# Optimization experiments

Hardware: AMD Instinct MI355X
Metric: run time of the kernel (lower is better)

## Reference

```python
import jax, jax.numpy as jnp
import numpy as np

TAU = 1.0
EPS = 1e-8  # F.cosine_similarity eps


def _cl(X, Y):
    # Pairwise cosine similarity via L2-normalize + single GEMM (N,D)@(D,N)
    Xn = X / jnp.maximum(jnp.linalg.norm(X, axis=1, keepdims=True), EPS)
    Yn = Y / jnp.maximum(jnp.linalg.norm(Y, axis=1, keepdims=True), EPS)
    sim = Xn @ Yn.T  # [N, N], sim[i, j] = cos(X_i, Y_j)
    e = jnp.exp(sim / TAU)
    pos = jnp.diagonal(e)               # exp(diag(sim)/tau), [N]
    neg = jnp.sum(e, axis=0) - pos      # column sums minus positive, [N]
    return -jnp.log(pos / neg).reshape(X.shape[0], 1)


def setup_inputs() -> dict:
    key = jax.random.key(0)
    ks = jax.random.split(key, 6)
    N, D1, D2, DO = 8192, 1024, 768, 256
    X = jax.random.normal(ks[0], (N, D1), dtype=jnp.float32)
    Y = jax.random.normal(ks[1], (N, D2), dtype=jnp.float32)
    # nn.Linear params (kaiming-uniform-ish scale)
    Wx = jax.random.uniform(ks[2], (DO, D1), jnp.float32, -1, 1) / np.sqrt(D1)
    bx = jax.random.uniform(ks[3], (DO,), jnp.float32, -1, 1) / np.sqrt(D1)
    Wy = jax.random.uniform(ks[4], (DO, D2), jnp.float32, -1, 1) / np.sqrt(D2)
    by = jax.random.uniform(ks[5], (DO,), jnp.float32, -1, 1) / np.sqrt(D2)
    return {"X": X, "Y": Y, "Wx": Wx, "bx": bx, "Wy": Wy, "by": by}


def reference(X, Y, Wx, bx, Wy, by):
    Xp = X @ Wx.T + bx  # proj_x
    Yp = Y @ Wy.T + by  # proj_y
    return _cl(Xp, Yp) + _cl(Yp, Xp)  # [N, 1]
```

## Files before the change

kernel.cpp:

```cpp
#include <hip/hip_runtime.h>
#include <hip/hip_bf16.h>

typedef __bf16 bf16_t;
typedef __bf16 bf16x8 __attribute__((ext_vector_type(8)));
typedef float  f32x4  __attribute__((ext_vector_type(4)));
typedef int    i32x8  __attribute__((ext_vector_type(8)));

__device__ __forceinline__ bf16x8 pack8(f32x4 a, f32x4 b) {
    bf16x8 h = { (bf16_t)a.x, (bf16_t)a.y, (bf16_t)a.z, (bf16_t)a.w,
                 (bf16_t)b.x, (bf16_t)b.y, (bf16_t)b.z, (bf16_t)b.w };
    return h;
}

__device__ __forceinline__ void gl_lds16(const void* g, void* l) {
    __builtin_amdgcn_global_load_lds(
        (const __attribute__((address_space(1))) unsigned int*)g,
        (__attribute__((address_space(3))) unsigned int*)l, 16, 0, 0);
}

#if __has_builtin(__builtin_amdgcn_cvt_pk_fp8_f32)
__device__ __forceinline__ unsigned char cvt1_e4m3(float x) {
    return (unsigned char)(__builtin_amdgcn_cvt_pk_fp8_f32(x, x, 0, false) & 0xff);
}
#else
__device__ __forceinline__ unsigned char cvt1_e4m3(float x) {
    unsigned u = __float_as_uint(x);
    unsigned sign = (u >> 24) & 0x80u;
    float a = fabsf(x);
    if (a < 7.8125e-3f) { int q = (int)(a * 512.0f + 0.5f); return (unsigned char)(sign | q); }
    if (a >= 448.0f) return (unsigned char)(sign | 0x7E);
    unsigned au = u & 0x7FFFFFFFu;
    unsigned lsb = (au >> 20) & 1u;
    au += 0x7FFFFu + lsb;
    int exp = (int)(au >> 23) - 127;
    unsigned man = (au >> 20) & 7u;
    return (unsigned char)(sign | ((unsigned)(exp + 7) << 3) | man);
}
#endif

__device__ __forceinline__ int frag_off_k(int row16, int k) {
    return ((k >> 6) << 10) + (((k >> 3) & 3) << 8) + (row16 << 4)
         + (((k >> 5) & 1) << 3) + (k & 7);
}

__global__ __launch_bounds__(256) void wconv(
    const float* __restrict__ Wx, const float* __restrict__ Wy,
    bf16_t* __restrict__ Wxt, bf16_t* __restrict__ Wyt)
{
    int id = blockIdx.x * 256 + threadIdx.x;

    int row, k0, K;
    const float* W;
    bf16_t* Wt;
    if (id < 32768) { W = Wx; Wt = Wxt; K = 1024; row = id >> 7; k0 = (id & 127) << 3; }
    else { int c = id - 32768; W = Wy; Wt = Wyt; K = 768; row = c / 96; k0 = (c % 96) << 3; }

    f32x4 lo = *reinterpret_cast<const f32x4*>(&W[(size_t)row * K + k0]);
    f32x4 hi = *reinterpret_cast<const f32x4*>(&W[(size_t)row * K + k0 + 4]);
    size_t off = (size_t)(row >> 4) * 16 * K + frag_off_k(row & 15, k0);
    *reinterpret_cast<bf16x8*>(Wt + off) = pack8(lo, hi);
}

__global__ __launch_bounds__(512, 2) void proj_norm(
    const float* __restrict__ X, const float* __restrict__ Y,
    const bf16_t* __restrict__ Wxt, const float* __restrict__ bxp,
    const bf16_t* __restrict__ Wyt, const float* __restrict__ byp,
    unsigned char* __restrict__ Xt, unsigned char* __restrict__ Yt)
{
    __shared__ float Abuf[2][64 * 64];
    __shared__ unsigned char obuf[16384];
    __shared__ float ssqL[4][64];

    const int tid  = threadIdx.x;
    const int lane = tid & 63;
    const int wave = tid >> 6;
    const int quad = lane >> 4;
    const int c16  = lane & 15;
    const int rg   = wave >> 2;
    const int cg   = wave & 3;

    const bool isY = blockIdx.x >= 128;
    const float*  A    = isY ? Y   : X;
    const bf16_t* Wt   = isY ? Wyt : Wxt;
    const float*  bias = isY ? byp : bxp;
    unsigned char* dst = isY ? Yt  : Xt;
    const int K = isY ? 768 : 1024;
    const int S = K >> 6;
    const int rowBase = (blockIdx.x & 127) * 64;

    auto stage = [&](int s, int b) {
        #pragma unroll
        for (int t = 0; t < 2; ++t) {
            int r0  = (wave * 2 + t) * 4;
            int row = r0 + (lane >> 4);
            int gch = (lane & 15) ^ (row & 15);
            gl_lds16(&A[(size_t)(rowBase + row) * K + s * 64 + gch * 4],
                     &Abuf[b][r0 * 64]);
        }
    };

    auto aFrag = [&](int b, int mf, int s2) -> bf16x8 {
        int row = rg * 32 + mf * 16 + c16;
        int e   = s2 * 8 + quad * 2;
        const float* base = &Abuf[b][row * 64];
        f32x4 lo = *reinterpret_cast<const f32x4*>(base + ((e ^ c16) << 2));
        f32x4 hi = *reinterpret_cast<const f32x4*>(base + (((e + 1) ^ c16) << 2));
        return pack8(lo, hi);
    };

    const bf16_t* pB[4];
    #pragma unroll
    for (int nf = 0; nf < 4; ++nf)
        pB[nf] = Wt + (size_t)(cg * 4 + nf) * 16 * K + quad * 256 + c16 * 16;

    f32x4 acc[2][4] = {};
    stage(0, 0);

    for (int s = 0; s < S; ++s) {
        const int b = s & 1;
        __syncthreads();
        if (s + 1 < S) stage(s + 1, b ^ 1);
        #pragma unroll
        for (int s2 = 0; s2 < 2; ++s2) {
            bf16x8 bF[4];
            #pragma unroll
            for (int nf = 0; nf < 4; ++nf)
                bF[nf] = *reinterpret_cast<const bf16x8*>(pB[nf] + s * 1024 + s2 * 8);
            #pragma unroll
            for (int mf = 0; mf < 2; ++mf) {
                bf16x8 aF = aFrag(b, mf, s2);
                #pragma unroll
                for (int nf = 0; nf < 4; ++nf)
                    acc[mf][nf] = __builtin_amdgcn_mfma_f32_16x16x32_bf16(
                        aF, bF[nf], acc[mf][nf], 0, 0, 0);
            }
        }
    }

    #pragma unroll
    for (int nf = 0; nf < 4; ++nf) {
        float bb = bias[cg * 64 + nf * 16 + c16];
        #pragma unroll
        for (int mf = 0; mf < 2; ++mf)
            #pragma unroll
            for (int r = 0; r < 4; ++r) acc[mf][nf][r] += bb;
    }

    #pragma unroll
    for (int mf = 0; mf < 2; ++mf)
        #pragma unroll
        for (int r = 0; r < 4; ++r) {
            float v = 0.f;
            #pragma unroll
            for (int nf = 0; nf < 4; ++nf) v += acc[mf][nf][r] * acc[mf][nf][r];
            v += __shfl_xor(v, 1, 64);
            v += __shfl_xor(v, 2, 64);
            v += __shfl_xor(v, 4, 64);
            v += __shfl_xor(v, 8, 64);
            if (c16 == 0) ssqL[cg][rg * 32 + mf * 16 + quad * 4 + r] = v;
        }
    __syncthreads();

    #pragma unroll
    for (int mf = 0; mf < 2; ++mf)
        #pragma unroll
        for (int r = 0; r < 4; ++r) {
            int lr = rg * 32 + mf * 16 + quad * 4 + r;
            float t = ssqL[0][lr] + ssqL[1][lr] + ssqL[2][lr] + ssqL[3][lr];
            float inv = 1.0f / fmaxf(sqrtf(t), 1e-8f);
            #pragma unroll
            for (int nf = 0; nf < 4; ++nf) {
                int k = cg * 64 + nf * 16 + c16;
                obuf[((lr >> 4) << 12) + ((k >> 5) << 9) + ((lr & 15) << 5) + (k & 31)] =
                    cvt1_e4m3(acc[mf][nf][r] * inv);
            }
        }
    __syncthreads();

    const f32x4* src = reinterpret_cast<const f32x4*>(&obuf[tid * 32]);
    f32x4* g = reinterpret_cast<f32x4*>(dst + (size_t)rowBase * 256 + tid * 32);
    g[0] = src[0];
    g[1] = src[1];
}

__global__ __launch_bounds__(256, 2) void sim_gemm(
    const unsigned char* __restrict__ Xt, const unsigned char* __restrict__ Yt,
    float* __restrict__ rowsumP, float* __restrict__ colsumP,
    float* __restrict__ pos)
{
    const int tid  = threadIdx.x;
    const int lane = tid & 63;
    const int wave = tid >> 6;
    const int quad = lane >> 4;
    const int c16  = lane & 15;
    const int wy   = wave >> 1;
    const int wx   = wave & 1;

    const int id = blockIdx.x;
    const int b2 = id >> 3;
    const int colBlk = (id & 7) * 8 + (b2 >> 4);
    const int rowGrp = b2 & 15;
    const int colBase = colBlk * 128;

    i32x8 B0[4], B1[4];
    #pragma unroll
    for (int nf = 0; nf < 4; ++nf) {
        const i32x8* p = reinterpret_cast<const i32x8*>(
            Yt + (size_t)(colBase + wx * 64 + nf * 16) * 256 + quad * 512 + c16 * 32);
        B0[nf] = p[0];
        B1[nf] = p[64];
    }

    auto aPtr = [&](int rowBase, int mf) {
        return reinterpret_cast<const i32x8*>(
            Xt + (size_t)(rowBase + wy * 64 + mf * 16) * 256 + quad * 512 + c16 * 32);
    };

    i32x8 A0[4], A1[4];
    #pragma unroll
    for (int mf = 0; mf < 4; ++mf) {
        const i32x8* p = aPtr(rowGrp * 512, mf);
        A0[mf] = p[0];
        A1[mf] = p[64];
    }

    float cs[4] = {0.f, 0.f, 0.f, 0.f};

    for (int t = 0; t < 4; ++t) {
        const int rowBase = rowGrp * 512 + t * 128;

        f32x4 acc[4][4] = {};
        __builtin_amdgcn_s_setprio(1);
        #pragma unroll
        for (int mf = 0; mf < 4; ++mf)
            #pragma unroll
            for (int nf = 0; nf < 4; ++nf)
                acc[mf][nf] = __builtin_amdgcn_mfma_scale_f32_16x16x128_f8f6f4(
                    A0[mf], B0[nf], acc[mf][nf], 0, 0, 0, 127, 0, 127);
        #pragma unroll
        for (int mf = 0; mf < 4; ++mf)
            #pragma unroll
            for (int nf = 0; nf < 4; ++nf)
                acc[mf][nf] = __builtin_amdgcn_mfma_scale_f32_16x16x128_f8f6f4(
                    A1[mf], B1[nf], acc[mf][nf], 0, 0, 0, 127, 0, 127);
        __builtin_amdgcn_s_setprio(0);

        if (t < 3) {
            #pragma unroll
            for (int mf = 0; mf < 4; ++mf) {
                const i32x8* p = aPtr(rowBase + 128, mf);
                A0[mf] = p[0];
                A1[mf] = p[64];
            }
        }

        #pragma unroll
        for (int mf = 0; mf < 4; ++mf)
            #pragma unroll
            for (int nf = 0; nf < 4; ++nf)
                #pragma unroll
                for (int r = 0; r < 4; ++r)
                    acc[mf][nf][r] = __expf(acc[mf][nf][r]);

        if (rowBase == colBase) {
            #pragma unroll
            for (int mf = 0; mf < 4; ++mf)
                #pragma unroll
                for (int nf = 0; nf < 4; ++nf)
                    #pragma unroll
                    for (int r = 0; r < 4; ++r) {
                        int lrow = wy * 64 + mf * 16 + quad * 4 + r;
                        int lcol = wx * 64 + nf * 16 + c16;
                        if (lrow == lcol) pos[rowBase + lrow] = acc[mf][nf][r];
                    }
        }

        float rs[4][4];
        #pragma unroll
        for (int mf = 0; mf < 4; ++mf)
            #pragma unroll
            for (int r = 0; r < 4; ++r) {
                float v = acc[mf][0][r] + acc[mf][1][r] + acc[mf][2][r] + acc[mf][3][r];
                v += __shfl_xor(v, 1, 64);
                v += __shfl_xor(v, 2, 64);
                v += __shfl_xor(v, 4, 64);
                v += __shfl_xor(v, 8, 64);
                rs[mf][r] = v;
            }

        float vsel = rs[0][0];
        #pragma unroll
        for (int k = 1; k < 16; ++k)
            vsel = (c16 == k) ? rs[k >> 2][k & 3] : vsel;
        int srcLane = ((lane >> 2) & 3) * 16 + (lane >> 4) * 4 + (lane & 3);
        float rowv = __shfl(vsel, srcLane, 64);
        rowsumP[(size_t)(colBlk * 2 + wx) * 8192 + rowBase + wy * 64 + lane] = rowv;

        #pragma unroll
        for (int nf = 0; nf < 4; ++nf) {
            float v = 0.f;
            #pragma unroll
            for (int mf = 0; mf < 4; ++mf)
                #pragma unroll
                for (int r = 0; r < 4; ++r)
                    v += acc[mf][nf][r];
            cs[nf] += v;
        }
    }

    #pragma unroll
    for (int nf = 0; nf < 4; ++nf) {
        float v = cs[nf];
        v += __shfl_xor(v, 16, 64);
        v += __shfl_xor(v, 32, 64);
        cs[nf] = v;
    }
    float csel = cs[0];
    #pragma unroll
    for (int k = 1; k < 4; ++k)
        csel = (quad == k) ? cs[k] : csel;
    colsumP[(size_t)(rowGrp * 2 + wy) * 8192 + colBase + wx * 64 + lane] = csel;
}

__global__ __launch_bounds__(256) void finalize(
    const float* __restrict__ rowsumP, const float* __restrict__ colsumP,
    const float* __restrict__ pos, float* __restrict__ out)
{
    int i = blockIdx.x * 256 + threadIdx.x;

    float r0 = 0.f, r1 = 0.f, r2 = 0.f, r3 = 0.f;
    #pragma unroll
    for (int c = 0; c < 128; c += 4) {
        r0 += rowsumP[(size_t)(c + 0) * 8192 + i];
        r1 += rowsumP[(size_t)(c + 1) * 8192 + i];
        r2 += rowsumP[(size_t)(c + 2) * 8192 + i];
        r3 += rowsumP[(size_t)(c + 3) * 8192 + i];
    }
    float rsum = (r0 + r1) + (r2 + r3);

    float c0 = 0.f, c1 = 0.f, c2 = 0.f, c3 = 0.f;
    #pragma unroll
    for (int g = 0; g < 32; g += 4) {
        c0 += colsumP[(size_t)(g + 0) * 8192 + i];
        c1 += colsumP[(size_t)(g + 1) * 8192 + i];
        c2 += colsumP[(size_t)(g + 2) * 8192 + i];
        c3 += colsumP[(size_t)(g + 3) * 8192 + i];
    }
    float csum = (c0 + c1) + (c2 + c3);

    float p = pos[i];
    out[i] = logf(csum - p) + logf(rsum - p) - 2.0f * logf(p);
}

extern "C" void kernel_launch(void* const* d_in, const int* in_sizes, int n_in,
                              void* d_out, int out_size, void* d_ws, size_t ws_size,
                              hipStream_t stream) {
    const float* X  = (const float*)d_in[0];
    const float* Y  = (const float*)d_in[1];
    const float* Wx = (const float*)d_in[2];
    const float* bx = (const float*)d_in[3];
    const float* Wy = (const float*)d_in[4];
    const float* by = (const float*)d_in[5];
    float* out = (float*)d_out;

    char* ws = (char*)d_ws;
    unsigned char* Xt  = (unsigned char*)(ws);
    unsigned char* Yt  = (unsigned char*)(ws + (2u << 20));
    bf16_t*        Wxt = (bf16_t*)(ws + (4u << 20));
    bf16_t*        Wyt = (bf16_t*)(ws + (4u << 20) + (512u << 10));
    float* rowsumP = (float*)(ws + (5u << 20));
    float* colsumP = (float*)(ws + (9u << 20));
    float* pos     = (float*)(ws + (10u << 20));

    wconv<<<224, 256, 0, stream>>>(Wx, Wy, Wxt, Wyt);
    proj_norm<<<256, 512, 0, stream>>>(X, Y, Wxt, bx, Wyt, by, Xt, Yt);
    sim_gemm<<<1024, 256, 0, stream>>>(Xt, Yt, rowsumP, colsumP, pos);
    finalize<<<32, 256, 0, stream>>>(rowsumP, colsumP, pos, out);
}
```

Measured before the change: 169.7 us.

## Interleave MFMA, A-prefetch and exp epilogue per row fragment; widen finalize grid

The sim_gemm inner tile loop is restructured so each row fragment's MFMAs are followed by that fragment's A prefetch and by the exp/reduction epilogue of the previous fragment, with sched_barriers enforcing the order. This lets the exp and shuffle work on the VALU overlap with matrix-core work instead of running after all 32 MFMAs. Column-sum accumulation is folded into the per-fragment epilogue. Separately, finalize now launches 256 blocks, splitting each output's partial-sum reduction across 8 thread groups and combining them in LDS, which gives more parallelism for the memory-bound reduction. The manual scheduling and full unrolling may raise register pressure.

```diff
diff --git a/kernel.cpp b/kernel.cpp
--- a/kernel.cpp
+++ b/kernel.cpp
@@ -226,45 +226,40 @@
 
     float cs[4] = {0.f, 0.f, 0.f, 0.f};
 
+    #pragma unroll
     for (int t = 0; t < 4; ++t) {
         const int rowBase = rowGrp * 512 + t * 128;
+        const bool diag = (rowBase == colBase);
 
         f32x4 acc[4][4] = {};
-        __builtin_amdgcn_s_setprio(1);
-        #pragma unroll
-        for (int mf = 0; mf < 4; ++mf)
+        float rs[4][4];
+
+        auto MFMA8 = [&](int mf) {
+            __builtin_amdgcn_s_setprio(1);
             #pragma unroll
             for (int nf = 0; nf < 4; ++nf)
                 acc[mf][nf] = __builtin_amdgcn_mfma_scale_f32_16x16x128_f8f6f4(
                     A0[mf], B0[nf], acc[mf][nf], 0, 0, 0, 127, 0, 127);
-        #pragma unroll
-        for (int mf = 0; mf < 4; ++mf)
             #pragma unroll
             for (int nf = 0; nf < 4; ++nf)
                 acc[mf][nf] = __builtin_amdgcn_mfma_scale_f32_16x16x128_f8f6f4(
                     A1[mf], B1[nf], acc[mf][nf], 0, 0, 0, 127, 0, 127);
-        __builtin_amdgcn_s_setprio(0);
-
-        if (t < 3) {
-            #pragma unroll
-            for (int mf = 0; mf < 4; ++mf) {
+            __builtin_amdgcn_s_setprio(0);
+        };
+        auto PF = [&](int mf) {
+            if (t < 3) {
                 const i32x8* p = aPtr(rowBase + 128, mf);
                 A0[mf] = p[0];
                 A1[mf] = p[64];
             }
-        }
-
-        #pragma unroll
-        for (int mf = 0; mf < 4; ++mf)
+        };
+        auto EPI = [&](int mf) {
             #pragma unroll
             for (int nf = 0; nf < 4; ++nf)
                 #pragma unroll
                 for (int r = 0; r < 4; ++r)
                     acc[mf][nf][r] = __expf(acc[mf][nf][r]);
-
-        if (rowBase == colBase) {
-            #pragma unroll
-            for (int mf = 0; mf < 4; ++mf)
+            if (diag) {
                 #pragma unroll
                 for (int nf = 0; nf < 4; ++nf)
                     #pragma unroll
@@ -273,11 +268,7 @@
                         int lcol = wx * 64 + nf * 16 + c16;
                         if (lrow == lcol) pos[rowBase + lrow] = acc[mf][nf][r];
                     }
-        }
-
-        float rs[4][4];
-        #pragma unroll
-        for (int mf = 0; mf < 4; ++mf)
+            }
             #pragma unroll
             for (int r = 0; r < 4; ++r) {
                 float v = acc[mf][0][r] + acc[mf][1][r] + acc[mf][2][r] + acc[mf][3][r];
@@ -287,6 +278,31 @@
                 v += __shfl_xor(v, 8, 64);
                 rs[mf][r] = v;
             }
+            #pragma unroll
+            for (int nf = 0; nf < 4; ++nf)
+                cs[nf] += (acc[mf][nf][0] + acc[mf][nf][1])
+                        + (acc[mf][nf][2] + acc[mf][nf][3]);
+        };
+
+        MFMA8(0);
+        __builtin_amdgcn_sched_barrier(0);
+        PF(0);
+        MFMA8(1);
+        __builtin_amdgcn_sched_barrier(0);
+        EPI(0);
+        __builtin_amdgcn_sched_barrier(0);
+        PF(1);
+        MFMA8(2);
+        __builtin_amdgcn_sched_barrier(0);
+        EPI(1);
+        __builtin_amdgcn_sched_barrier(0);
+        PF(2);
+        MFMA8(3);
+        __builtin_amdgcn_sched_barrier(0);
+        EPI(2);
+        __builtin_amdgcn_sched_barrier(0);
+        PF(3);
+        EPI(3);
 
         float vsel = rs[0][0];
         #pragma unroll
@@ -295,17 +311,6 @@
         int srcLane = ((lane >> 2) & 3) * 16 + (lane >> 4) * 4 + (lane & 3);
         float rowv = __shfl(vsel, srcLane, 64);
         rowsumP[(size_t)(colBlk * 2 + wx) * 8192 + rowBase + wy * 64 + lane] = rowv;
-
-        #pragma unroll
-        for (int nf = 0; nf < 4; ++nf) {
-            float v = 0.f;
-            #pragma unroll
-            for (int mf = 0; mf < 4; ++mf)
-                #pragma unroll
-                for (int r = 0; r < 4; ++r)
-                    v += acc[mf][nf][r];
-            cs[nf] += v;
-        }
     }
 
     #pragma unroll
@@ -326,30 +331,36 @@
     const float* __restrict__ rowsumP, const float* __restrict__ colsumP,
     const float* __restrict__ pos, float* __restrict__ out)
 {
-    int i = blockIdx.x * 256 + threadIdx.x;
-
-    float r0 = 0.f, r1 = 0.f, r2 = 0.f, r3 = 0.f;
-    #pragma unroll
-    for (int c = 0; c < 128; c += 4) {
-        r0 += rowsumP[(size_t)(c + 0) * 8192 + i];
-        r1 += rowsumP[(size_t)(c + 1) * 8192 + i];
-        r2 += rowsumP[(size_t)(c + 2) * 8192 + i];
-        r3 += rowsumP[(size_t)(c + 3) * 8192 + i];
-    }
-    float rsum = (r0 + r1) + (r2 + r3);
-
-    float c0 = 0.f, c1 = 0.f, c2 = 0.f, c3 = 0.f;
-    #pragma unroll
-    for (int g = 0; g < 32; g += 4) {
-        c0 += colsumP[(size_t)(g + 0) * 8192 + i];
-        c1 += colsumP[(size_t)(g + 1) * 8192 + i];
-        c2 += colsumP[(size_t)(g + 2) * 8192 + i];
-        c3 += colsumP[(size_t)(g + 3) * 8192 + i];
-    }
-    float csum = (c0 + c1) + (c2 + c3);
-
-    float p = pos[i];
-    out[i] = logf(csum - p) + logf(rsum - p) - 2.0f * logf(p);
+    __shared__ float redR[256], redC[256];
+
+    const int oi   = threadIdx.x & 31;
+    const int part = threadIdx.x >> 5;
+    const int i    = blockIdx.x * 32 + oi;
+
+    float r = 0.f;
+    #pragma unroll
+    for (int c = part; c < 128; c += 8)
+        r += rowsumP[(size_t)c * 8192 + i];
+
+    float cv = 0.f;
+    #pragma unroll
+    for (int g = part; g < 32; g += 8)
+        cv += colsumP[(size_t)g * 8192 + i];
+
+    redR[threadIdx.x] = r;
+    redC[threadIdx.x] = cv;
+    __syncthreads();
+
+    if (threadIdx.x < 32) {
+        float rsum = 0.f, csum = 0.f;
+        #pragma unroll
+        for (int p = 0; p < 8; ++p) {
+            rsum += redR[oi + 32 * p];
+            csum += redC[oi + 32 * p];
+        }
+        float p = pos[i];
+        out[i] = logf(csum - p) + logf(rsum - p) - 2.0f * logf(p);
+    }
 }
 
 extern "C" void kernel_launch(void* const* d_in, const int* in_sizes, int n_in,
@@ -375,5 +386,5 @@
     wconv<<<224, 256, 0, stream>>>(Wx, Wy, Wxt, Wyt);
     proj_norm<<<256, 512, 0, stream>>>(X, Y, Wxt, bx, Wyt, by, Xt, Yt);
     sim_gemm<<<1024, 256, 0, stream>>>(Xt, Yt, rowsumP, colsumP, pos);
-    finalize<<<32, 256, 0, stream>>>(rowsumP, colsumP, pos, out);
-}
+    finalize<<<256, 256, 0, stream>>>(rowsumP, colsumP, pos, out);
+}
```

Result: slower. 189.1 us (+11.4%).

## Hold A tile resident and stream B tiles; parallelize finalize reduction

Applied to the files above, without the earlier changes.

The similarity GEMM now keeps each block's 128-row X tile in registers and walks four 128-column Y tiles, instead of keeping the Y tile and walking rows. Row sums accumulate across iterations and are reduced once at the end, while column partials are written per tile, so rowsumP shrinks to 32 partials and colsumP grows to 128. The finalize kernel splits each output's partial reduction across 8 threads with an LDS combine and launches 256 blocks instead of 32, so more of the GPU takes part in that small tail pass. The trade is more column-partial traffic from the GEMM in exchange for fewer per-iteration row shuffles and a better-parallelized finalize.

```diff
diff --git a/kernel.cpp b/kernel.cpp
--- a/kernel.cpp
+++ b/kernel.cpp
@@ -196,38 +196,38 @@
     const int wy   = wave >> 1;
     const int wx   = wave & 1;
 
-    const int id = blockIdx.x;
-    const int b2 = id >> 3;
-    const int colBlk = (id & 7) * 8 + (b2 >> 4);
-    const int rowGrp = b2 & 15;
-    const int colBase = colBlk * 128;
+    const int id  = blockIdx.x;
+    const int idx = id >> 3;
+    const int colGrp = ((idx >> 6) << 3) + (id & 7);
+    const int rowBlk = idx & 63;
+    const int rowBase = rowBlk * 128;
+
+    i32x8 A0[4], A1[4];
+    #pragma unroll
+    for (int mf = 0; mf < 4; ++mf) {
+        const i32x8* p = reinterpret_cast<const i32x8*>(
+            Xt + (size_t)(rowBase + wy * 64 + mf * 16) * 256 + quad * 512 + c16 * 32);
+        A0[mf] = p[0];
+        A1[mf] = p[64];
+    }
+
+    auto bPtr = [&](int cBase, int nf) {
+        return reinterpret_cast<const i32x8*>(
+            Yt + (size_t)(cBase + wx * 64 + nf * 16) * 256 + quad * 512 + c16 * 32);
+    };
 
     i32x8 B0[4], B1[4];
     #pragma unroll
     for (int nf = 0; nf < 4; ++nf) {
-        const i32x8* p = reinterpret_cast<const i32x8*>(
-            Yt + (size_t)(colBase + wx * 64 + nf * 16) * 256 + quad * 512 + c16 * 32);
+        const i32x8* p = bPtr(colGrp * 512, nf);
         B0[nf] = p[0];
         B1[nf] = p[64];
     }
 
-    auto aPtr = [&](int rowBase, int mf) {
-        return reinterpret_cast<const i32x8*>(
-            Xt + (size_t)(rowBase + wy * 64 + mf * 16) * 256 + quad * 512 + c16 * 32);
-    };
-
-    i32x8 A0[4], A1[4];
-    #pragma unroll
-    for (int mf = 0; mf < 4; ++mf) {
-        const i32x8* p = aPtr(rowGrp * 512, mf);
-        A0[mf] = p[0];
-        A1[mf] = p[64];
-    }
-
-    float cs[4] = {0.f, 0.f, 0.f, 0.f};
+    f32x4 rr[4] = {};
 
     for (int t = 0; t < 4; ++t) {
-        const int rowBase = rowGrp * 512 + t * 128;
+        const int cBase = colGrp * 512 + t * 128;
 
         f32x4 acc[4][4] = {};
         __builtin_amdgcn_s_setprio(1);
@@ -247,10 +247,10 @@
 
         if (t < 3) {
             #pragma unroll
-            for (int mf = 0; mf < 4; ++mf) {
-                const i32x8* p = aPtr(rowBase + 128, mf);
-                A0[mf] = p[0];
-                A1[mf] = p[64];
+            for (int nf = 0; nf < 4; ++nf) {
+                const i32x8* p = bPtr(cBase + 128, nf);
+                B0[nf] = p[0];
+                B1[nf] = p[64];
             }
         }
 
@@ -262,7 +262,7 @@
                 for (int r = 0; r < 4; ++r)
                     acc[mf][nf][r] = __expf(acc[mf][nf][r]);
 
-        if (rowBase == colBase) {
+        if (rowBase == cBase) {
             #pragma unroll
             for (int mf = 0; mf < 4; ++mf)
                 #pragma unroll
@@ -275,81 +275,81 @@
                     }
         }
 
-        float rs[4][4];
+        float cst[4];
+        #pragma unroll
+        for (int nf = 0; nf < 4; ++nf) {
+            f32x4 tv = (acc[0][nf] + acc[1][nf]) + (acc[2][nf] + acc[3][nf]);
+            float s = (tv[0] + tv[1]) + (tv[2] + tv[3]);
+            s += __shfl_xor(s, 16, 64);
+            s += __shfl_xor(s, 32, 64);
+            cst[nf] = s;
+        }
+        float csel = cst[0];
+        #pragma unroll
+        for (int k = 1; k < 4; ++k)
+            csel = (quad == k) ? cst[k] : csel;
+        colsumP[(size_t)(rowBlk * 2 + wy) * 8192 + cBase + wx * 64 + lane] = csel;
+
         #pragma unroll
         for (int mf = 0; mf < 4; ++mf)
-            #pragma unroll
-            for (int r = 0; r < 4; ++r) {
-                float v = acc[mf][0][r] + acc[mf][1][r] + acc[mf][2][r] + acc[mf][3][r];
-                v += __shfl_xor(v, 1, 64);
-                v += __shfl_xor(v, 2, 64);
-                v += __shfl_xor(v, 4, 64);
-                v += __shfl_xor(v, 8, 64);
-                rs[mf][r] = v;
-            }
-
-        float vsel = rs[0][0];
-        #pragma unroll
-        for (int k = 1; k < 16; ++k)
-            vsel = (c16 == k) ? rs[k >> 2][k & 3] : vsel;
-        int srcLane = ((lane >> 2) & 3) * 16 + (lane >> 4) * 4 + (lane & 3);
-        float rowv = __shfl(vsel, srcLane, 64);
-        rowsumP[(size_t)(colBlk * 2 + wx) * 8192 + rowBase + wy * 64 + lane] = rowv;
-
-        #pragma unroll
-        for (int nf = 0; nf < 4; ++nf) {
-            float v = 0.f;
-            #pragma unroll
-            for (int mf = 0; mf < 4; ++mf)
-                #pragma unroll
-                for (int r = 0; r < 4; ++r)
-                    v += acc[mf][nf][r];
-            cs[nf] += v;
-        }
-    }
-
-    #pragma unroll
-    for (int nf = 0; nf < 4; ++nf) {
-        float v = cs[nf];
-        v += __shfl_xor(v, 16, 64);
-        v += __shfl_xor(v, 32, 64);
-        cs[nf] = v;
-    }
-    float csel = cs[0];
-    #pragma unroll
-    for (int k = 1; k < 4; ++k)
-        csel = (quad == k) ? cs[k] : csel;
-    colsumP[(size_t)(rowGrp * 2 + wy) * 8192 + colBase + wx * 64 + lane] = csel;
+            rr[mf] += (acc[mf][0] + acc[mf][1]) + (acc[mf][2] + acc[mf][3]);
+    }
+
+    float rs[4][4];
+    #pragma unroll
+    for (int mf = 0; mf < 4; ++mf)
+        #pragma unroll
+        for (int r = 0; r < 4; ++r) {
+            float v = rr[mf][r];
+            v += __shfl_xor(v, 1, 64);
+            v += __shfl_xor(v, 2, 64);
+            v += __shfl_xor(v, 4, 64);
+            v += __shfl_xor(v, 8, 64);
+            rs[mf][r] = v;
+        }
+    float vsel = rs[0][0];
+    #pragma unroll
+    for (int k = 1; k < 16; ++k)
+        vsel = (c16 == k) ? rs[k >> 2][k & 3] : vsel;
+    int srcLane = ((lane >> 2) & 3) * 16 + (lane >> 4) * 4 + (lane & 3);
+    float rowv = __shfl(vsel, srcLane, 64);
+    rowsumP[(size_t)(colGrp * 2 + wx) * 8192 + rowBase + wy * 64 + lane] = rowv;
 }
 
 __global__ __launch_bounds__(256) void finalize(
     const float* __restrict__ rowsumP, const float* __restrict__ colsumP,
     const float* __restrict__ pos, float* __restrict__ out)
 {
-    int i = blockIdx.x * 256 + threadIdx.x;
-
-    float r0 = 0.f, r1 = 0.f, r2 = 0.f, r3 = 0.f;
-    #pragma unroll
-    for (int c = 0; c < 128; c += 4) {
-        r0 += rowsumP[(size_t)(c + 0) * 8192 + i];
-        r1 += rowsumP[(size_t)(c + 1) * 8192 + i];
-        r2 += rowsumP[(size_t)(c + 2) * 8192 + i];
-        r3 += rowsumP[(size_t)(c + 3) * 8192 + i];
-    }
-    float rsum = (r0 + r1) + (r2 + r3);
-
-    float c0 = 0.f, c1 = 0.f, c2 = 0.f, c3 = 0.f;
-    #pragma unroll
-    for (int g = 0; g < 32; g += 4) {
-        c0 += colsumP[(size_t)(g + 0) * 8192 + i];
-        c1 += colsumP[(size_t)(g + 1) * 8192 + i];
-        c2 += colsumP[(size_t)(g + 2) * 8192 + i];
-        c3 += colsumP[(size_t)(g + 3) * 8192 + i];
-    }
-    float csum = (c0 + c1) + (c2 + c3);
-
-    float p = pos[i];
-    out[i] = logf(csum - p) + logf(rsum - p) - 2.0f * logf(p);
+    __shared__ float redR[256], redC[256];
+
+    const int oi   = threadIdx.x & 31;
+    const int part = threadIdx.x >> 5;
+    const int i    = blockIdx.x * 32 + oi;
+
+    float r = 0.f;
+    #pragma unroll
+    for (int c = part; c < 32; c += 8)
+        r += rowsumP[(size_t)c * 8192 + i];
+
+    float cv = 0.f;
+    #pragma unroll
+    for (int g = part; g < 128; g += 8)
+        cv += colsumP[(size_t)g * 8192 + i];
+
+    redR[threadIdx.x] = r;
+    redC[threadIdx.x] = cv;
+    __syncthreads();
+
+    if (threadIdx.x < 32) {
+        float rsum = 0.f, csum = 0.f;
+        #pragma unroll
+        for (int p = 0; p < 8; ++p) {
+            rsum += redR[oi + 32 * p];
+            csum += redC[oi + 32 * p];
+        }
+        float p = pos[i];
+        out[i] = logf(csum - p) + logf(rsum - p) - 2.0f * logf(p);
+    }
 }
 
 extern "C" void kernel_launch(void* const* d_in, const int* in_sizes, int n_in,
@@ -369,11 +369,11 @@
     bf16_t*        Wxt = (bf16_t*)(ws + (4u << 20));
     bf16_t*        Wyt = (bf16_t*)(ws + (4u << 20) + (512u << 10));
     float* rowsumP = (float*)(ws + (5u << 20));
-    float* colsumP = (float*)(ws + (9u << 20));
+    float* colsumP = (float*)(ws + (6u << 20));
     float* pos     = (float*)(ws + (10u << 20));
 
     wconv<<<224, 256, 0, stream>>>(Wx, Wy, Wxt, Wyt);
     proj_norm<<<256, 512, 0, stream>>>(X, Y, Wxt, bx, Wyt, by, Xt, Yt);
     sim_gemm<<<1024, 256, 0, stream>>>(Xt, Yt, rowsumP, colsumP, pos);
-    finalize<<<32, 256, 0, stream>>>(rowsumP, colsumP, pos, out);
-}
+    finalize<<<256, 256, 0, stream>>>(rowsumP, colsumP, pos, out);
+}
```

After: 184.2 us. +8.5%, slower.
